# Kernel optimization log

Hardware: AMD Instinct MI355X
Metric: run time of the kernel (lower is better)

The kernel has to match this reference:

```python
import jax, jax.numpy as jnp
import numpy as np

WS = 8      # window_size
SS = 4      # shift_size
DIM = 192
HEADS = 6
N = WS * WS
EPS = 1e-5


def _rel_pos_index():
    coords = np.stack(np.meshgrid(np.arange(WS), np.arange(WS), indexing='ij')).reshape(2, -1)
    rel = (coords[:, :, None] - coords[:, None, :]).transpose(1, 2, 0)  # [N,N,2]
    rel[..., 0] += WS - 1
    rel[..., 1] += WS - 1
    rel[..., 0] *= 2 * WS - 1
    return rel.sum(-1)  # [N,N] int


def _attn_mask(H, W):
    img = np.zeros((H, W))
    sl = (slice(0, -WS), slice(-WS, -SS), slice(-SS, None))
    cnt = 0
    for hs in sl:
        for ws_ in sl:
            img[hs, ws_] = cnt
            cnt += 1
    mw = img.reshape(H // WS, WS, W // WS, WS).transpose(0, 2, 1, 3).reshape(-1, N)
    d = mw[:, None, :] - mw[:, :, None]
    return np.where(d != 0, -100.0, 0.0).astype(np.float32)  # [nW,N,N]


def _ln(x, g, b):
    m = x.mean(-1, keepdims=True)
    v = ((x - m) ** 2).mean(-1, keepdims=True)
    return (x - m) / jnp.sqrt(v + EPS) * g + b


def setup_inputs() -> dict:
    key = jax.random.key(0)
    ks = jax.random.split(key, 12)
    C, Hd = DIM, DIM * 4
    s = 0.02
    return {
        'x': jax.random.normal(ks[0], (2, 256, 256, C), dtype=jnp.float32),
        'norm1_g': jnp.ones((C,), jnp.float32),
        'norm1_b': jnp.zeros((C,), jnp.float32),
        'qkv_w': jax.random.normal(ks[1], (3 * C, C), jnp.float32) * s,
        'rpb_table': jax.random.normal(ks[2], ((2 * WS - 1) ** 2, HEADS), jnp.float32) * s,
        'proj_w': jax.random.normal(ks[3], (C, C), jnp.float32) * s,
        'proj_b': jnp.zeros((C,), jnp.float32),
        'norm2_g': jnp.ones((C,), jnp.float32),
        'norm2_b': jnp.zeros((C,), jnp.float32),
        'mlp_w1': jax.random.normal(ks[4], (Hd, C), jnp.float32) * s,
        'mlp_b1': jnp.zeros((Hd,), jnp.float32),
        'mlp_w2': jax.random.normal(ks[5], (C, Hd), jnp.float32) * s,
        'mlp_b2': jnp.zeros((C,), jnp.float32),
    }


def reference(x, norm1_g, norm1_b, qkv_w, rpb_table, proj_w, proj_b,
              norm2_g, norm2_b, mlp_w1, mlp_b1, mlp_w2, mlp_b2):
    B, H, W, C = x.shape
    hd = C // HEADS
    shortcut = x
    xn = _ln(x, norm1_g, norm1_b)
    xs = jnp.roll(xn, (-SS, -SS), axis=(1, 2))
    # window partition -> [B_*nW, N, C]
    xw = xs.reshape(B, H // WS, WS, W // WS, WS, C).transpose(0, 1, 3, 2, 4, 5).reshape(-1, N, C)
    B_ = xw.shape[0]
    qkv = (xw @ qkv_w.T).reshape(B_, N, 3, HEADS, hd).transpose(2, 0, 3, 1, 4)
    q, k, v = qkv[0] * (hd ** -0.5), qkv[1], qkv[2]
    attn = jnp.einsum('bhid,bhjd->bhij', q, k)  # [B_,H,N,N]
    rpi = jnp.asarray(_rel_pos_index().reshape(-1))
    bias = rpb_table[rpi].reshape(N, N, HEADS).transpose(2, 0, 1)  # [H,N,N]
    attn = attn + bias[None]
    mask = jnp.asarray(_attn_mask(H, W))  # [nW,N,N]
    nW = mask.shape[0]
    attn = (attn.reshape(B_ // nW, nW, HEADS, N, N) + mask[None, :, None]).reshape(B_, HEADS, N, N)
    attn = jax.nn.softmax(attn, axis=-1)
    out = jnp.einsum('bhij,bhjd->bhid', attn, v).transpose(0, 2, 1, 3).reshape(B_, N, C)
    out = out @ proj_w.T + proj_b
    # window reverse + roll back
    out = out.reshape(B, H // WS, W // WS, WS, WS, C).transpose(0, 1, 3, 2, 4, 5).reshape(B, H, W, C)
    x1 = shortcut + jnp.roll(out, (SS, SS), axis=(1, 2))
    h = _ln(x1, norm2_g, norm2_b)
    h = jax.nn.gelu(h @ mlp_w1.T + mlp_b1, approximate=False)
    h = h @ mlp_w2.T + mlp_b2
    return x1 + h
```

## Files before the change

### kernel.cpp

```cpp
#include <hip/hip_runtime.h>
#include <hip/hip_bf16.h>
#include <math.h>

typedef unsigned short u16;
typedef unsigned int u32;
typedef __attribute__((ext_vector_type(8))) short short8;
typedef __attribute__((ext_vector_type(4))) float floatx4;

__device__ __forceinline__ float bf2f(u16 u) { return __uint_as_float(((u32)u) << 16); }
__device__ __forceinline__ u16 f2bf(float f) {
  u32 u = __float_as_uint(f);
  u32 r = u + 0x7fffu + ((u >> 16) & 1u);
  return (u16)(r >> 16);
}

#define WSB_OFF  0
#define WSQ_OFF  393216
#define WSP_OFF  614400
#define WSM1_OFF 688128
#define WSM2_OFF 983040

__global__ __launch_bounds__(256) void k_prep(
    const float* __restrict__ qkvw, const float* __restrict__ projw,
    const float* __restrict__ rpb,
    const float* __restrict__ w1, const float* __restrict__ w2,
    float* __restrict__ wsb, u16* __restrict__ wsq, u16* __restrict__ wsp,
    u16* __restrict__ wsm1, u16* __restrict__ wsm2)
{
  const int tid0 = blockIdx.x * 256 + threadIdx.x;
  const int NT = gridDim.x * 256;
  for (int idx = tid0; idx < 110592; idx += NT) {
    int e = idx & 7, lane = (idx >> 3) & 63, rest = idx >> 9;
    int s = rest % 6, T = rest / 6;
    int mat = T / 12, hct = T % 12;
    int row = mat * 192 + hct * 16 + (lane & 15);
    int col = 32 * s + 8 * (lane >> 4) + e;
    float v = qkvw[(size_t)row * 192 + col];
    if (mat == 0) v *= 0.1767766952966369f;
    wsq[idx] = f2bf(v);
  }
  for (int idx = tid0; idx < 36864; idx += NT) {
    int e = idx & 7, lane = (idx >> 3) & 63, rest = idx >> 9;
    int nt = rest % 12, h = rest / 12;
    int row = 16 * nt + (lane & 15);
    int col = 32 * h + 8 * (lane >> 4) + e;
    wsp[idx] = f2bf(projw[(size_t)row * 192 + col]);
  }
  for (int idx = tid0; idx < 147456; idx += NT) {
    int e = idx & 7, lane = (idx >> 3) & 63, rest = idx >> 9;
    int s = rest % 6, t = rest / 6;
    int n = t & 1, ch = t >> 1;
    wsm1[idx] = f2bf(w1[(size_t)(ch * 32 + n * 16 + (lane & 15)) * 192
                        + 32 * s + 8 * (lane >> 4) + e]);
  }
  for (int idx = tid0; idx < 147456; idx += NT) {
    int e = idx & 7, lane = (idx >> 3) & 63, rest = idx >> 9;
    int ct = rest % 12, ch = rest / 12;
    wsm2[idx] = f2bf(w2[(size_t)(ct * 16 + (lane & 15)) * 768
                        + ch * 32 + 8 * (lane >> 4) + e]);
  }
  for (int idx = tid0; idx < 98304; idx += NT) {
    int f16 = idx & 15; int nt = f16 >> 2, r = f16 & 3;
    int t = (idx >> 4) & 255; int rest = idx >> 12;
    int h = rest % 6, cat = rest / 6;
    int w = t >> 6, m = t & 15, ql = (t >> 4) & 3;
    int i = 16 * w + 4 * ql + r, j = 16 * nt + m;
    int ir = i >> 3, ic = i & 7, jr = j >> 3, jc = j & 7;
    float v = rpb[((ir - jr + 7) * 15 + (ic - jc + 7)) * 6 + h];
    int catH = cat >> 1, catW = cat & 1;
    int ci = (catH ? ((ir < 4) ? 1 : 2) : 0) * 3 + (catW ? ((ic < 4) ? 1 : 2) : 0);
    int cj = (catH ? ((jr < 4) ? 1 : 2) : 0) * 3 + (catW ? ((jc < 4) ? 1 : 2) : 0);
    if (ci != cj) v -= 100.f;
    wsb[idx] = v;
  }
}

__global__ __launch_bounds__(256) void k_attn(
    const float* __restrict__ x,
    const float* __restrict__ g1, const float* __restrict__ b1,
    const float* __restrict__ projb,
    const float* __restrict__ wsb, const u16* __restrict__ wsq,
    const u16* __restrict__ wsp,
    float* __restrict__ out)
{
  __shared__ __align__(16) u16 xn[64][200];
  __shared__ __align__(16) u16 qs[64][40];
  __shared__ __align__(16) u16 ks[64][40];
  __shared__ __align__(16) u16 vT[32][72];
  __shared__ __align__(16) u16 PO[4608];

  const int tid = threadIdx.x;
  const int blk = blockIdx.x;
  const int b  = blk >> 10;
  const int wh = (blk >> 5) & 31;
  const int ww = blk & 31;

  {
    const int t = tid >> 2, l4 = tid & 3;
    const int rr = t >> 3, cc = t & 7;
    const int oh = (wh * 8 + rr + 4) & 255;
    const int ow = (ww * 8 + cc + 4) & 255;
    const float* px = x + (((size_t)b * 65536 + (size_t)oh * 256 + ow) * 192) + l4 * 48;
    float rv[48];
    float s = 0.f, ss = 0.f;
    const float4* p4 = (const float4*)px;
    #pragma unroll
    for (int i = 0; i < 12; ++i) {
      float4 v = p4[i];
      rv[i*4+0] = v.x; rv[i*4+1] = v.y; rv[i*4+2] = v.z; rv[i*4+3] = v.w;
      s  += v.x + v.y + v.z + v.w;
      ss += v.x*v.x + v.y*v.y + v.z*v.z + v.w*v.w;
    }
    s += __shfl_xor(s, 1);  s += __shfl_xor(s, 2);
    ss += __shfl_xor(ss, 1); ss += __shfl_xor(ss, 2);
    const float mean = s * (1.f / 192.f);
    const float var  = ss * (1.f / 192.f) - mean * mean;
    const float rstd = rsqrtf(var + 1e-5f);
    const int c0 = l4 * 48;
    #pragma unroll
    for (int i = 0; i < 12; ++i) {
      ushort4 o;
      o.x = f2bf((rv[i*4+0] - mean) * rstd * g1[c0+i*4+0] + b1[c0+i*4+0]);
      o.y = f2bf((rv[i*4+1] - mean) * rstd * g1[c0+i*4+1] + b1[c0+i*4+1]);
      o.z = f2bf((rv[i*4+2] - mean) * rstd * g1[c0+i*4+2] + b1[c0+i*4+2]);
      o.w = f2bf((rv[i*4+3] - mean) * rstd * g1[c0+i*4+3] + b1[c0+i*4+3]);
      *(ushort4*)&xn[t][c0 + i*4] = o;
    }
  }

  const int w    = tid >> 6;
  const int lane = tid & 63;
  const int m    = tid & 15;
  const int ql   = (tid >> 4) & 3;
  const int ct   = w >> 1;
  const int tb   = (w & 1) * 2;
  const int cat  = ((wh == 31) ? 2 : 0) | ((ww == 31) ? 1 : 0);
  const float* pbias = wsb + ((size_t)(cat * 6) * 256 + tid) * 16;
  const int po = w * 1152;

  floatx4 acc[12];
  #pragma unroll
  for (int nt = 0; nt < 12; ++nt) acc[nt] = (floatx4){0.f, 0.f, 0.f, 0.f};

  __syncthreads();

  #pragma unroll 1
  for (int h = 0; h < 6; ++h) {
    {
      const u16* wqp = wsq + (size_t)(h * 2 + ct) * 3072 + lane * 8;
      floatx4 dq[2], dk[2], dv[2];
      #pragma unroll
      for (int t = 0; t < 2; ++t) {
        dq[t] = (floatx4){0.f,0.f,0.f,0.f};
        dk[t] = (floatx4){0.f,0.f,0.f,0.f};
        dv[t] = (floatx4){0.f,0.f,0.f,0.f};
      }
      #pragma unroll
      for (int s = 0; s < 6; ++s) {
        short8 a0 = *(const short8*)&xn[16*tb + m][32*s + 8*ql];
        short8 a1 = *(const short8*)&xn[16*tb + 16 + m][32*s + 8*ql];
        short8 bq = *(const short8*)(wqp + s*512);
        short8 bk = *(const short8*)(wqp + 36864 + s*512);
        short8 bv = *(const short8*)(wqp + 73728 + s*512);
        dq[0] = __builtin_amdgcn_mfma_f32_16x16x32_bf16(a0, bq, dq[0], 0, 0, 0);
        dq[1] = __builtin_amdgcn_mfma_f32_16x16x32_bf16(a1, bq, dq[1], 0, 0, 0);
        dk[0] = __builtin_amdgcn_mfma_f32_16x16x32_bf16(a0, bk, dk[0], 0, 0, 0);
        dk[1] = __builtin_amdgcn_mfma_f32_16x16x32_bf16(a1, bk, dk[1], 0, 0, 0);
        dv[0] = __builtin_amdgcn_mfma_f32_16x16x32_bf16(a0, bv, dv[0], 0, 0, 0);
        dv[1] = __builtin_amdgcn_mfma_f32_16x16x32_bf16(a1, bv, dv[1], 0, 0, 0);
      }
      #pragma unroll
      for (int t = 0; t < 2; ++t) {
        #pragma unroll
        for (int r = 0; r < 4; ++r) {
          qs[16*(tb+t) + 4*ql + r][ct*16 + m] = f2bf(dq[t][r]);
          ks[16*(tb+t) + 4*ql + r][ct*16 + m] = f2bf(dk[t][r]);
        }
        ushort4 o;
        o.x = f2bf(dv[t][0]); o.y = f2bf(dv[t][1]);
        o.z = f2bf(dv[t][2]); o.w = f2bf(dv[t][3]);
        *(ushort4*)&vT[ct*16 + m][16*(tb+t) + 4*ql] = o;
      }
    }
    __syncthreads();

    floatx4 sf[4];
    {
      short8 aq = *(const short8*)&qs[16*w + m][8*ql];
      const float* pb = pbias + (size_t)h * 4096;
      #pragma unroll
      for (int nt = 0; nt < 4; ++nt) {
        float4 b4 = *(const float4*)(pb + nt*4);
        short8 bk = *(const short8*)&ks[16*nt + m][8*ql];
        sf[nt] = __builtin_amdgcn_mfma_f32_16x16x32_bf16(
            aq, bk, (floatx4){b4.x, b4.y, b4.z, b4.w}, 0, 0, 0);
      }
    }
    {
      float mxr[4] = {-3.0e38f, -3.0e38f, -3.0e38f, -3.0e38f};
      #pragma unroll
      for (int nt = 0; nt < 4; ++nt)
        #pragma unroll
        for (int r = 0; r < 4; ++r) mxr[r] = fmaxf(mxr[r], sf[nt][r]);
      #pragma unroll
      for (int d = 1; d <= 8; d <<= 1)
        #pragma unroll
        for (int r = 0; r < 4; ++r) mxr[r] = fmaxf(mxr[r], __shfl_xor(mxr[r], d));
      float smr[4] = {0.f, 0.f, 0.f, 0.f};
      #pragma unroll
      for (int nt = 0; nt < 4; ++nt)
        #pragma unroll
        for (int r = 0; r < 4; ++r) {
          float e = __expf(sf[nt][r] - mxr[r]);
          sf[nt][r] = e;
          smr[r] += e;
        }
      #pragma unroll
      for (int d = 1; d <= 8; d <<= 1)
        #pragma unroll
        for (int r = 0; r < 4; ++r) smr[r] += __shfl_xor(smr[r], d);
      #pragma unroll
      for (int r = 0; r < 4; ++r) {
        const float inv = 1.f / smr[r];
        #pragma unroll
        for (int nt = 0; nt < 4; ++nt)
          PO[po + (4*ql + r)*72 + 16*nt + m] = f2bf(sf[nt][r] * inv);
      }
    }

    floatx4 of[2];
    of[0] = (floatx4){0.f,0.f,0.f,0.f}; of[1] = (floatx4){0.f,0.f,0.f,0.f};
    #pragma unroll
    for (int s = 0; s < 2; ++s) {
      short8 ap = *(const short8*)&PO[po + m*72 + 32*s + 8*ql];
      #pragma unroll
      for (int mt = 0; mt < 2; ++mt) {
        short8 bv = *(const short8*)&vT[16*mt + m][32*s + 8*ql];
        of[mt] = __builtin_amdgcn_mfma_f32_16x16x32_bf16(ap, bv, of[mt], 0, 0, 0);
      }
    }
    __syncthreads();

    #pragma unroll
    for (int mt = 0; mt < 2; ++mt)
      #pragma unroll
      for (int r = 0; r < 4; ++r)
        PO[po + (4*ql + r)*40 + 16*mt + m] = f2bf(of[mt][r]);
    {
      short8 ao = *(const short8*)&PO[po + m*40 + 8*ql];
      const u16* wpp = wsp + (size_t)h * 6144 + lane * 8;
      #pragma unroll
      for (int nt = 0; nt < 12; ++nt) {
        short8 bw = *(const short8*)(wpp + nt*512);
        acc[nt] = __builtin_amdgcn_mfma_f32_16x16x32_bf16(ao, bw, acc[nt], 0, 0, 0);
      }
    }
  }

  {
    size_t rbase[4];
    #pragma unroll
    for (int r = 0; r < 4; ++r) {
      const int i  = 16*w + 4*ql + r;
      const int ir = i >> 3, ic = i & 7;
      const int oh = (wh * 8 + ir + 4) & 255;
      const int ow = (ww * 8 + ic + 4) & 255;
      rbase[r] = ((size_t)b * 65536 + (size_t)oh * 256 + ow) * 192;
    }
    #pragma unroll
    for (int nt = 0; nt < 12; ++nt) {
      const int c = 16*nt + m;
      const float pb = projb[c];
      #pragma unroll
      for (int r = 0; r < 4; ++r) {
        const size_t idx = rbase[r] + c;
        out[idx] = x[idx] + acc[nt][r] + pb;
      }
    }
  }
}

__global__ __launch_bounds__(256) void k_mlp(
    const float* __restrict__ g2, const float* __restrict__ b2,
    const u16* __restrict__ wsm1, const float* __restrict__ bm1,
    const u16* __restrict__ wsm2, const float* __restrict__ bm2,
    float* __restrict__ io)
{
  __shared__ __align__(16) u16 shbuf[12800];
  __shared__ u16 gs[4][16][40];

  const int tid = threadIdx.x;
  const size_t tok0 = (size_t)blockIdx.x * 64;

  const int w = tid >> 6;
  const int lane = tid & 63;
  const int m = lane & 15;
  const int q = lane >> 4;

  short8 pf1[3];
  {
    const u16* p1 = wsm1;
    #pragma unroll
    for (int it = 0; it < 3; ++it)
      pf1[it] = *(const short8*)(p1 + (it * 256 + tid) * 8);
  }

  {
    const int t = tid >> 2, l4 = tid & 3;
    const float* px = io + (tok0 + t) * 192 + l4 * 48;
    float rv[48];
    float s = 0.f, ss = 0.f;
    const float4* p4 = (const float4*)px;
    #pragma unroll
    for (int i = 0; i < 12; ++i) {
      float4 v = p4[i];
      rv[i*4+0] = v.x; rv[i*4+1] = v.y; rv[i*4+2] = v.z; rv[i*4+3] = v.w;
      s += v.x + v.y + v.z + v.w;
      ss += v.x*v.x + v.y*v.y + v.z*v.z + v.w*v.w;
    }
    s += __shfl_xor(s, 1);  s += __shfl_xor(s, 2);
    ss += __shfl_xor(ss, 1); ss += __shfl_xor(ss, 2);
    const float mean = s * (1.f / 192.f);
    const float var  = ss * (1.f / 192.f) - mean * mean;
    const float rstd = rsqrtf(var + 1e-5f);
    const int c0 = l4 * 48;
    #pragma unroll
    for (int i = 0; i < 12; ++i) {
      ushort4 o;
      o.x = f2bf((rv[i*4+0] - mean) * rstd * g2[c0+i*4+0] + b2[c0+i*4+0]);
      o.y = f2bf((rv[i*4+1] - mean) * rstd * g2[c0+i*4+1] + b2[c0+i*4+1]);
      o.z = f2bf((rv[i*4+2] - mean) * rstd * g2[c0+i*4+2] + b2[c0+i*4+2]);
      o.w = f2bf((rv[i*4+3] - mean) * rstd * g2[c0+i*4+3] + b2[c0+i*4+3]);
      *(ushort4*)&shbuf[t * 200 + c0 + i*4] = o;
    }
  }
  __syncthreads();

  short8 a_all[6];
  #pragma unroll
  for (int s = 0; s < 6; ++s)
    a_all[s] = *(const short8*)&shbuf[(16 * w + m) * 200 + 32 * s + 8 * q];
  __syncthreads();

  #pragma unroll
  for (int it = 0; it < 3; ++it)
    *(short8*)&shbuf[(it * 256 + tid) * 8] = pf1[it];
  {
    const u16* p1 = wsm1 + 6144;
    #pragma unroll
    for (int it = 0; it < 3; ++it)
      pf1[it] = *(const short8*)(p1 + (it * 256 + tid) * 8);
  }
  __syncthreads();

  floatx4 c2acc[12];
  #pragma unroll
  for (int ct = 0; ct < 12; ++ct) c2acc[ct] = (floatx4){0.f, 0.f, 0.f, 0.f};

  #pragma unroll 1
  for (int ch = 0; ch < 24; ++ch) {
    const int buf = ch & 1;

    short8 w2r[12];
    {
      const u16* w2p = wsm2 + (size_t)ch * 6144 + lane * 8;
      #pragma unroll
      for (int ct = 0; ct < 12; ++ct)
        w2r[ct] = *(const short8*)(w2p + ct * 512);
    }

    const u16* w1p = shbuf + buf * 6144 + lane * 8;
    floatx4 h0 = (floatx4){0.f, 0.f, 0.f, 0.f};
    floatx4 h1 = (floatx4){0.f, 0.f, 0.f, 0.f};
    #pragma unroll
    for (int s = 0; s < 6; ++s) {
      short8 b0 = *(const short8*)(w1p + s * 512);
      short8 b1 = *(const short8*)(w1p + 3072 + s * 512);
      h0 = __builtin_amdgcn_mfma_f32_16x16x32_bf16(a_all[s], b0, h0, 0, 0, 0);
      h1 = __builtin_amdgcn_mfma_f32_16x16x32_bf16(a_all[s], b1, h1, 0, 0, 0);
    }

    const int c0 = ch * 32;
    {
      const float bb0 = bm1[c0 + m];
      const float bb1 = bm1[c0 + 16 + m];
      #pragma unroll
      for (int r = 0; r < 4; ++r) {
        float v0 = h0[r] + bb0;
        float v1 = h1[r] + bb1;
        float g0 = 0.5f * v0 * (1.f + erff(v0 * 0.70710678118654752f));
        float g1 = 0.5f * v1 * (1.f + erff(v1 * 0.70710678118654752f));
        gs[w][q * 4 + r][m] = f2bf(g0);
        gs[w][q * 4 + r][16 + m] = f2bf(g1);
      }
    }

    {
      short8 ap = *(const short8*)&gs[w][m][8 * q];
      #pragma unroll
      for (int ct = 0; ct < 12; ++ct)
        c2acc[ct] = __builtin_amdgcn_mfma_f32_16x16x32_bf16(ap, w2r[ct], c2acc[ct], 0, 0, 0);
    }

    if (ch + 1 < 24) {
      #pragma unroll
      for (int it = 0; it < 3; ++it)
        *(short8*)&shbuf[(buf ^ 1) * 6144 + (it * 256 + tid) * 8] = pf1[it];
      if (ch + 2 < 24) {
        const u16* p1 = wsm1 + (size_t)(ch + 2) * 6144;
        #pragma unroll
        for (int it = 0; it < 3; ++it)
          pf1[it] = *(const short8*)(p1 + (it * 256 + tid) * 8);
      }
      __syncthreads();
    }
  }

  #pragma unroll
  for (int ct = 0; ct < 12; ++ct) {
    const int c = ct * 16 + m;
    const float bb = bm2[c];
    #pragma unroll
    for (int r = 0; r < 4; ++r) {
      const size_t idx = (tok0 + 16 * w + q * 4 + r) * 192 + c;
      io[idx] = c2acc[ct][r] + bb + io[idx];
    }
  }
}

extern "C" void kernel_launch(void* const* d_in, const int* in_sizes, int n_in,
                              void* d_out, int out_size, void* d_ws, size_t ws_size,
                              hipStream_t stream) {
  (void)in_sizes; (void)n_in; (void)out_size; (void)ws_size;
  const float* x    = (const float*)d_in[0];
  const float* n1g  = (const float*)d_in[1];
  const float* n1b  = (const float*)d_in[2];
  const float* qkvw = (const float*)d_in[3];
  const float* rpb  = (const float*)d_in[4];
  const float* pw   = (const float*)d_in[5];
  const float* pb   = (const float*)d_in[6];
  const float* n2g  = (const float*)d_in[7];
  const float* n2b  = (const float*)d_in[8];
  const float* w1   = (const float*)d_in[9];
  const float* bm1  = (const float*)d_in[10];
  const float* w2   = (const float*)d_in[11];
  const float* bm2  = (const float*)d_in[12];
  float* out = (float*)d_out;

  float* wsb  = (float*)((char*)d_ws + WSB_OFF);
  u16*   wsq  = (u16*)((char*)d_ws + WSQ_OFF);
  u16*   wsp  = (u16*)((char*)d_ws + WSP_OFF);
  u16*   wsm1 = (u16*)((char*)d_ws + WSM1_OFF);
  u16*   wsm2 = (u16*)((char*)d_ws + WSM2_OFF);

  hipLaunchKernelGGL(k_prep, dim3(192), dim3(256), 0, stream,
                     qkvw, pw, rpb, w1, w2, wsb, wsq, wsp, wsm1, wsm2);
  hipLaunchKernelGGL(k_attn, dim3(2048), dim3(256), 0, stream,
                     x, n1g, n1b, pb, wsb, wsq, wsp, out);
  hipLaunchKernelGGL(k_mlp, dim3(2048), dim3(256), 0, stream,
                     n2g, n2b, wsm1, bm1, wsm2, bm2, out);
}
```

Before: 498.1 us.

## Fuse window attention and MLP into one kernel keeping residual in registers

```diff
diff --git a/kernel.cpp b/kernel.cpp
--- a/kernel.cpp
+++ b/kernel.cpp
@@ -75,19 +75,20 @@
   }
 }
 
-__global__ __launch_bounds__(256) void k_attn(
+__global__ __launch_bounds__(256, 4) void k_fused(
     const float* __restrict__ x,
     const float* __restrict__ g1, const float* __restrict__ b1,
     const float* __restrict__ projb,
     const float* __restrict__ wsb, const u16* __restrict__ wsq,
     const u16* __restrict__ wsp,
+    const float* __restrict__ g2, const float* __restrict__ b2,
+    const u16* __restrict__ wsm1, const float* __restrict__ bm1,
+    const u16* __restrict__ wsm2, const float* __restrict__ bm2,
     float* __restrict__ out)
 {
-  __shared__ __align__(16) u16 xn[64][200];
-  __shared__ __align__(16) u16 qs[64][40];
-  __shared__ __align__(16) u16 ks[64][40];
-  __shared__ __align__(16) u16 vT[32][72];
-  __shared__ __align__(16) u16 PO[4608];
+  __shared__ __align__(16) u16 xnA[12800];
+  __shared__ __align__(16) u16 pool[12288];
+  const int QS = 0, KS = 2560, VT = 5120, POB = 7424;
 
   const int tid = threadIdx.x;
   const int blk = blockIdx.x;
@@ -124,7 +125,7 @@
       o.y = f2bf((rv[i*4+1] - mean) * rstd * g1[c0+i*4+1] + b1[c0+i*4+1]);
       o.z = f2bf((rv[i*4+2] - mean) * rstd * g1[c0+i*4+2] + b1[c0+i*4+2]);
       o.w = f2bf((rv[i*4+3] - mean) * rstd * g1[c0+i*4+3] + b1[c0+i*4+3]);
-      *(ushort4*)&xn[t][c0 + i*4] = o;
+      *(ushort4*)&xnA[t * 200 + c0 + i*4] = o;
     }
   }
 
@@ -136,7 +137,7 @@
   const int tb   = (w & 1) * 2;
   const int cat  = ((wh == 31) ? 2 : 0) | ((ww == 31) ? 1 : 0);
   const float* pbias = wsb + ((size_t)(cat * 6) * 256 + tid) * 16;
-  const int po = w * 1152;
+  const int po = POB + w * 1152;
 
   floatx4 acc[12];
   #pragma unroll
@@ -157,8 +158,8 @@
       }
       #pragma unroll
       for (int s = 0; s < 6; ++s) {
-        short8 a0 = *(const short8*)&xn[16*tb + m][32*s + 8*ql];
-        short8 a1 = *(const short8*)&xn[16*tb + 16 + m][32*s + 8*ql];
+        short8 a0 = *(const short8*)&xnA[(16*tb + m) * 200 + 32*s + 8*ql];
+        short8 a1 = *(const short8*)&xnA[(16*tb + 16 + m) * 200 + 32*s + 8*ql];
         short8 bq = *(const short8*)(wqp + s*512);
         short8 bk = *(const short8*)(wqp + 36864 + s*512);
         short8 bv = *(const short8*)(wqp + 73728 + s*512);
@@ -173,25 +174,25 @@
       for (int t = 0; t < 2; ++t) {
         #pragma unroll
         for (int r = 0; r < 4; ++r) {
-          qs[16*(tb+t) + 4*ql + r][ct*16 + m] = f2bf(dq[t][r]);
-          ks[16*(tb+t) + 4*ql + r][ct*16 + m] = f2bf(dk[t][r]);
+          pool[QS + (16*(tb+t) + 4*ql + r)*40 + ct*16 + m] = f2bf(dq[t][r]);
+          pool[KS + (16*(tb+t) + 4*ql + r)*40 + ct*16 + m] = f2bf(dk[t][r]);
         }
         ushort4 o;
         o.x = f2bf(dv[t][0]); o.y = f2bf(dv[t][1]);
         o.z = f2bf(dv[t][2]); o.w = f2bf(dv[t][3]);
-        *(ushort4*)&vT[ct*16 + m][16*(tb+t) + 4*ql] = o;
+        *(ushort4*)&pool[VT + (ct*16 + m)*72 + 16*(tb+t) + 4*ql] = o;
       }
     }
     __syncthreads();
 
     floatx4 sf[4];
     {
-      short8 aq = *(const short8*)&qs[16*w + m][8*ql];
+      short8 aq = *(const short8*)&pool[QS + (16*w + m)*40 + 8*ql];
       const float* pb = pbias + (size_t)h * 4096;
       #pragma unroll
       for (int nt = 0; nt < 4; ++nt) {
         float4 b4 = *(const float4*)(pb + nt*4);
-        short8 bk = *(const short8*)&ks[16*nt + m][8*ql];
+        short8 bk = *(const short8*)&pool[KS + (16*nt + m)*40 + 8*ql];
         sf[nt] = __builtin_amdgcn_mfma_f32_16x16x32_bf16(
             aq, bk, (floatx4){b4.x, b4.y, b4.z, b4.w}, 0, 0, 0);
       }
@@ -224,7 +225,7 @@
         const float inv = 1.f / smr[r];
         #pragma unroll
         for (int nt = 0; nt < 4; ++nt)
-          PO[po + (4*ql + r)*72 + 16*nt + m] = f2bf(sf[nt][r] * inv);
+          pool[po + (4*ql + r)*72 + 16*nt + m] = f2bf(sf[nt][r] * inv);
       }
     }
 
@@ -232,10 +233,10 @@
     of[0] = (floatx4){0.f,0.f,0.f,0.f}; of[1] = (floatx4){0.f,0.f,0.f,0.f};
     #pragma unroll
     for (int s = 0; s < 2; ++s) {
-      short8 ap = *(const short8*)&PO[po + m*72 + 32*s + 8*ql];
+      short8 ap = *(const short8*)&pool[po + m*72 + 32*s + 8*ql];
       #pragma unroll
       for (int mt = 0; mt < 2; ++mt) {
-        short8 bv = *(const short8*)&vT[16*mt + m][32*s + 8*ql];
+        short8 bv = *(const short8*)&pool[VT + (16*mt + m)*72 + 32*s + 8*ql];
         of[mt] = __builtin_amdgcn_mfma_f32_16x16x32_bf16(ap, bv, of[mt], 0, 0, 0);
       }
     }
@@ -245,9 +246,9 @@
     for (int mt = 0; mt < 2; ++mt)
       #pragma unroll
       for (int r = 0; r < 4; ++r)
-        PO[po + (4*ql + r)*40 + 16*mt + m] = f2bf(of[mt][r]);
-    {
-      short8 ao = *(const short8*)&PO[po + m*40 + 8*ql];
+        pool[po + (4*ql + r)*40 + 16*mt + m] = f2bf(of[mt][r]);
+    {
+      short8 ao = *(const short8*)&pool[po + m*40 + 8*ql];
       const u16* wpp = wsp + (size_t)h * 6144 + lane * 8;
       #pragma unroll
       for (int nt = 0; nt < 12; ++nt) {
@@ -257,105 +258,80 @@
     }
   }
 
+  short8 pf1[3];
+  #pragma unroll
+  for (int it = 0; it < 3; ++it)
+    pf1[it] = *(const short8*)(wsm1 + (size_t)(it * 256 + tid) * 8);
+
+  size_t rbase[4];
+  #pragma unroll
+  for (int r = 0; r < 4; ++r) {
+    const int i  = 16*w + 4*ql + r;
+    const int ir = i >> 3, ic = i & 7;
+    const int oh = (wh * 8 + ir + 4) & 255;
+    const int ow = (ww * 8 + ic + 4) & 255;
+    rbase[r] = ((size_t)b * 65536 + (size_t)oh * 256 + ow) * 192;
+  }
+  floatx4 c2acc[12];
+  #pragma unroll
+  for (int nt = 0; nt < 12; ++nt) {
+    const int c = 16*nt + m;
+    const float pb = projb[c];
+    #pragma unroll
+    for (int r = 0; r < 4; ++r)
+      c2acc[nt][r] = x[rbase[r] + c] + acc[nt][r] + pb;
+  }
+
   {
-    size_t rbase[4];
+    float s[4] = {0.f,0.f,0.f,0.f}, ss[4] = {0.f,0.f,0.f,0.f};
+    #pragma unroll
+    for (int nt = 0; nt < 12; ++nt)
+      #pragma unroll
+      for (int r = 0; r < 4; ++r) {
+        float v = c2acc[nt][r];
+        s[r] += v; ss[r] += v * v;
+      }
+    #pragma unroll
+    for (int d = 1; d <= 8; d <<= 1)
+      #pragma unroll
+      for (int r = 0; r < 4; ++r) {
+        s[r]  += __shfl_xor(s[r], d);
+        ss[r] += __shfl_xor(ss[r], d);
+      }
+    float mean[4], rstd[4];
     #pragma unroll
     for (int r = 0; r < 4; ++r) {
-      const int i  = 16*w + 4*ql + r;
-      const int ir = i >> 3, ic = i & 7;
-      const int oh = (wh * 8 + ir + 4) & 255;
-      const int ow = (ww * 8 + ic + 4) & 255;
-      rbase[r] = ((size_t)b * 65536 + (size_t)oh * 256 + ow) * 192;
+      mean[r] = s[r] * (1.f / 192.f);
+      float var = ss[r] * (1.f / 192.f) - mean[r] * mean[r];
+      rstd[r] = rsqrtf(var + 1e-5f);
     }
     #pragma unroll
     for (int nt = 0; nt < 12; ++nt) {
       const int c = 16*nt + m;
-      const float pb = projb[c];
+      const float gg = g2[c], bb = b2[c], bb2 = bm2[c];
       #pragma unroll
       for (int r = 0; r < 4; ++r) {
-        const size_t idx = rbase[r] + c;
-        out[idx] = x[idx] + acc[nt][r] + pb;
-      }
-    }
-  }
-}
-
-__global__ __launch_bounds__(256) void k_mlp(
-    const float* __restrict__ g2, const float* __restrict__ b2,
-    const u16* __restrict__ wsm1, const float* __restrict__ bm1,
-    const u16* __restrict__ wsm2, const float* __restrict__ bm2,
-    float* __restrict__ io)
-{
-  __shared__ __align__(16) u16 shbuf[12800];
-  __shared__ u16 gs[4][16][40];
-
-  const int tid = threadIdx.x;
-  const size_t tok0 = (size_t)blockIdx.x * 64;
-
-  const int w = tid >> 6;
-  const int lane = tid & 63;
-  const int m = lane & 15;
-  const int q = lane >> 4;
-
-  short8 pf1[3];
-  {
-    const u16* p1 = wsm1;
-    #pragma unroll
-    for (int it = 0; it < 3; ++it)
-      pf1[it] = *(const short8*)(p1 + (it * 256 + tid) * 8);
-  }
-
-  {
-    const int t = tid >> 2, l4 = tid & 3;
-    const float* px = io + (tok0 + t) * 192 + l4 * 48;
-    float rv[48];
-    float s = 0.f, ss = 0.f;
-    const float4* p4 = (const float4*)px;
-    #pragma unroll
-    for (int i = 0; i < 12; ++i) {
-      float4 v = p4[i];
-      rv[i*4+0] = v.x; rv[i*4+1] = v.y; rv[i*4+2] = v.z; rv[i*4+3] = v.w;
-      s += v.x + v.y + v.z + v.w;
-      ss += v.x*v.x + v.y*v.y + v.z*v.z + v.w*v.w;
-    }
-    s += __shfl_xor(s, 1);  s += __shfl_xor(s, 2);
-    ss += __shfl_xor(ss, 1); ss += __shfl_xor(ss, 2);
-    const float mean = s * (1.f / 192.f);
-    const float var  = ss * (1.f / 192.f) - mean * mean;
-    const float rstd = rsqrtf(var + 1e-5f);
-    const int c0 = l4 * 48;
-    #pragma unroll
-    for (int i = 0; i < 12; ++i) {
-      ushort4 o;
-      o.x = f2bf((rv[i*4+0] - mean) * rstd * g2[c0+i*4+0] + b2[c0+i*4+0]);
-      o.y = f2bf((rv[i*4+1] - mean) * rstd * g2[c0+i*4+1] + b2[c0+i*4+1]);
-      o.z = f2bf((rv[i*4+2] - mean) * rstd * g2[c0+i*4+2] + b2[c0+i*4+2]);
-      o.w = f2bf((rv[i*4+3] - mean) * rstd * g2[c0+i*4+3] + b2[c0+i*4+3]);
-      *(ushort4*)&shbuf[t * 200 + c0 + i*4] = o;
-    }
-  }
+        xnA[(16*w + 4*ql + r) * 200 + c] = f2bf((c2acc[nt][r] - mean[r]) * rstd[r] * gg + bb);
+        c2acc[nt][r] += bb2;
+      }
+    }
+  }
+
+  short8 a_all[6];
+  #pragma unroll
+  for (int s = 0; s < 6; ++s)
+    a_all[s] = *(const short8*)&xnA[(16*w + m) * 200 + 32*s + 8*ql];
+
   __syncthreads();
-
-  short8 a_all[6];
-  #pragma unroll
-  for (int s = 0; s < 6; ++s)
-    a_all[s] = *(const short8*)&shbuf[(16 * w + m) * 200 + 32 * s + 8 * q];
+  #pragma unroll
+  for (int it = 0; it < 3; ++it)
+    *(short8*)&pool[(it * 256 + tid) * 8] = pf1[it];
+  #pragma unroll
+  for (int it = 0; it < 3; ++it)
+    pf1[it] = *(const short8*)(wsm1 + 6144 + (size_t)(it * 256 + tid) * 8);
   __syncthreads();
 
-  #pragma unroll
-  for (int it = 0; it < 3; ++it)
-    *(short8*)&shbuf[(it * 256 + tid) * 8] = pf1[it];
-  {
-    const u16* p1 = wsm1 + 6144;
-    #pragma unroll
-    for (int it = 0; it < 3; ++it)
-      pf1[it] = *(const short8*)(p1 + (it * 256 + tid) * 8);
-  }
-  __syncthreads();
-
-  floatx4 c2acc[12];
-  #pragma unroll
-  for (int ct = 0; ct < 12; ++ct) c2acc[ct] = (floatx4){0.f, 0.f, 0.f, 0.f};
+  const int gsb = w * 640;
 
   #pragma unroll 1
   for (int ch = 0; ch < 24; ++ch) {
@@ -365,11 +341,11 @@
     {
       const u16* w2p = wsm2 + (size_t)ch * 6144 + lane * 8;
       #pragma unroll
-      for (int ct = 0; ct < 12; ++ct)
-        w2r[ct] = *(const short8*)(w2p + ct * 512);
-    }
-
-    const u16* w1p = shbuf + buf * 6144 + lane * 8;
+      for (int ct2 = 0; ct2 < 12; ++ct2)
+        w2r[ct2] = *(const short8*)(w2p + ct2 * 512);
+    }
+
+    const u16* w1p = pool + buf * 6144 + lane * 8;
     floatx4 h0 = (floatx4){0.f, 0.f, 0.f, 0.f};
     floatx4 h1 = (floatx4){0.f, 0.f, 0.f, 0.f};
     #pragma unroll
@@ -390,22 +366,22 @@
         float v1 = h1[r] + bb1;
         float g0 = 0.5f * v0 * (1.f + erff(v0 * 0.70710678118654752f));
         float g1 = 0.5f * v1 * (1.f + erff(v1 * 0.70710678118654752f));
-        gs[w][q * 4 + r][m] = f2bf(g0);
-        gs[w][q * 4 + r][16 + m] = f2bf(g1);
-      }
-    }
-
-    {
-      short8 ap = *(const short8*)&gs[w][m][8 * q];
-      #pragma unroll
-      for (int ct = 0; ct < 12; ++ct)
-        c2acc[ct] = __builtin_amdgcn_mfma_f32_16x16x32_bf16(ap, w2r[ct], c2acc[ct], 0, 0, 0);
+        xnA[gsb + (ql * 4 + r) * 40 + m] = f2bf(g0);
+        xnA[gsb + (ql * 4 + r) * 40 + 16 + m] = f2bf(g1);
+      }
+    }
+
+    {
+      short8 ap = *(const short8*)&xnA[gsb + m * 40 + 8 * ql];
+      #pragma unroll
+      for (int ct2 = 0; ct2 < 12; ++ct2)
+        c2acc[ct2] = __builtin_amdgcn_mfma_f32_16x16x32_bf16(ap, w2r[ct2], c2acc[ct2], 0, 0, 0);
     }
 
     if (ch + 1 < 24) {
       #pragma unroll
       for (int it = 0; it < 3; ++it)
-        *(short8*)&shbuf[(buf ^ 1) * 6144 + (it * 256 + tid) * 8] = pf1[it];
+        *(short8*)&pool[(buf ^ 1) * 6144 + (it * 256 + tid) * 8] = pf1[it];
       if (ch + 2 < 24) {
         const u16* p1 = wsm1 + (size_t)(ch + 2) * 6144;
         #pragma unroll
@@ -417,14 +393,11 @@
   }
 
   #pragma unroll
-  for (int ct = 0; ct < 12; ++ct) {
-    const int c = ct * 16 + m;
-    const float bb = bm2[c];
-    #pragma unroll
-    for (int r = 0; r < 4; ++r) {
-      const size_t idx = (tok0 + 16 * w + q * 4 + r) * 192 + c;
-      io[idx] = c2acc[ct][r] + bb + io[idx];
-    }
+  for (int nt = 0; nt < 12; ++nt) {
+    const int c = 16*nt + m;
+    #pragma unroll
+    for (int r = 0; r < 4; ++r)
+      out[rbase[r] + c] = c2acc[nt][r];
   }
 }
 
@@ -455,8 +428,7 @@
 
   hipLaunchKernelGGL(k_prep, dim3(192), dim3(256), 0, stream,
                      qkvw, pw, rpb, w1, w2, wsb, wsq, wsp, wsm1, wsm2);
-  hipLaunchKernelGGL(k_attn, dim3(2048), dim3(256), 0, stream,
-                     x, n1g, n1b, pb, wsb, wsq, wsp, out);
-  hipLaunchKernelGGL(k_mlp, dim3(2048), dim3(256), 0, stream,
+  hipLaunchKernelGGL(k_fused, dim3(2048), dim3(256), 0, stream,
+                     x, n1g, n1b, pb, wsb, wsq, wsp,
                      n2g, n2b, wsm1, bm1, wsm2, bm2, out);
 }
```

Result: slower. 703.1 us (+41.2%).
